# Kernel tuning notes

Hardware: AMD Instinct MI355X
Metric: run time of the kernel (lower is better)

The kernel has to match this reference:

```python
import jax, jax.numpy as jnp
import numpy as np

B, T, D, U, O = 256, 512, 256, 512, 64  # batch, n_steps, feature_in, units, n_output


def setup_inputs() -> dict:
    key = jax.random.key(0)
    k_x, k_wx, k_wh, k_wd = jax.random.split(key, 4)
    x = jax.random.normal(k_x, (B, T, D), dtype=jnp.float32)
    # Lecun-normal-ish init scales so activations stay sane
    Wx = jax.random.normal(k_wx, (D, 4 * U), dtype=jnp.float32) * (1.0 / np.sqrt(D))
    Wh = jax.random.normal(k_wh, (U, 4 * U), dtype=jnp.float32) * (1.0 / np.sqrt(U))
    b = jnp.zeros((4 * U,), dtype=jnp.float32)
    Wd = jax.random.normal(k_wd, (U, O), dtype=jnp.float32) * (1.0 / np.sqrt(U))
    bd = jnp.zeros((O,), dtype=jnp.float32)
    return {"x": x, "Wx": Wx, "Wh": Wh, "b": b, "Wd": Wd, "bd": bd}


def reference(x, Wx, Wh, b, Wd, bd):
    """Sequential LSTM scan (flax nn.LSTMCell math) + per-step dense decode.

    x: [B, T, D] -> y: [B, T, O]
    """
    batch = x.shape[0]
    units = Wh.shape[0]
    c0 = jnp.zeros((batch, units), dtype=x.dtype)
    h0 = jnp.zeros((batch, units), dtype=x.dtype)

    def step(carry, xt):
        c, h = carry
        gates = xt @ Wx + h @ Wh + b            # [B, 4U]
        i, f, g, o = jnp.split(gates, 4, axis=-1)
        i = jax.nn.sigmoid(i)
        f = jax.nn.sigmoid(f)
        g = jnp.tanh(g)
        o = jax.nn.sigmoid(o)
        c_new = f * c + i * g
        h_new = o * jnp.tanh(c_new)
        y = h_new @ Wd + bd                     # [B, O]
        return (c_new, h_new), y

    xs = jnp.swapaxes(x, 0, 1)                  # [T, B, D]
    _, ys = jax.lax.scan(step, (c0, h0), xs)    # ys: [T, B, O]
    return jnp.swapaxes(ys, 0, 1)               # [B, T, O]
```

## Files before the change

kernel.cpp:

```cpp
#include <hip/hip_runtime.h>


#define Bb 256
#define Tt 512
#define Dd 256
#define Uu 512
#define Oo 64

typedef short bs8 __attribute__((ext_vector_type(8)));
typedef float f32x4 __attribute__((ext_vector_type(4)));

__device__ __forceinline__ unsigned short f2bf(float f) {
  unsigned u = __float_as_uint(f);
  u += 0x7fffu + ((u >> 16) & 1u);
  return (unsigned short)(u >> 16);
}
__device__ __forceinline__ float bf2f(unsigned short s) {
  return __uint_as_float(((unsigned)s) << 16);
}
__device__ __forceinline__ float sigm(float v) { return 1.0f / (1.0f + __expf(-v)); }
__device__ __forceinline__ float tanhfast(float v) { return 2.0f / (1.0f + __expf(-2.0f * v)) - 1.0f; }

__device__ __forceinline__ int zbyte(int row, int k) {
  return (row * 1536 + k * 2) ^ ((row & 7) << 4);
}

__global__ void rnn_init_bar(unsigned* bar) {
  __hip_atomic_store(&bar[threadIdx.x], 0u, __ATOMIC_RELAXED, __HIP_MEMORY_SCOPE_AGENT);
}

__launch_bounds__(256, 2)
__global__ void rnn_lstm_kernel(const float* __restrict__ x, const float* __restrict__ Wx,
                                const float* __restrict__ Wh, const float* __restrict__ bias,
                                const float* __restrict__ Wd, const float* __restrict__ bd,
                                float* __restrict__ out, unsigned short* hbuf, unsigned* bar) {
  __shared__ __align__(16) char zs[16 * 768 * 2];
  __shared__ float gates[4][16][17];
  __shared__ float wdl[512][2];
  __shared__ float ypart[16][2][16];

  const int tid = threadIdx.x;
  const int lane = tid & 63;
  const int wid = tid >> 6;
  const int bid = blockIdx.x;
  const int bg = (bid & 7) | ((bid >> 8) << 3);
  const int ug = (bid >> 3) & 31;
  const int b_base = bg * 16;
  const int u_base = ug * 16;
  const int oc0 = ug * 2;

  unsigned* fl = bar + bg * 32;

  bs8 breg[24];
  {
    const int gc = wid * 512 + u_base + (lane & 15);
    const int kfr = (lane >> 4) * 8;
#pragma unroll
    for (int ks = 0; ks < 24; ++ks) {
      bs8 bb;
#pragma unroll
      for (int e = 0; e < 8; ++e) {
        int kg = ks * 32 + kfr + e;
        float w = (kg < 256) ? Wx[(size_t)kg * 2048 + gc]
                             : Wh[(size_t)(kg - 256) * 2048 + gc];
        bb[e] = (short)f2bf(w);
      }
      breg[ks] = bb;
    }
  }

  const int prow = tid & 15;
  const int usec = tid >> 4;
  const int us4 = usec & 3;
  float bi[4], bff[4], bgg[4], boo[4];
  if (tid < 64) {
#pragma unroll
    for (int j = 0; j < 4; ++j) {
      int ugl = u_base + us4 * 4 + j;
      bi[j]  = bias[0 * 512 + ugl];
      bff[j] = bias[1 * 512 + ugl];
      bgg[j] = bias[2 * 512 + ugl];
      boo[j] = bias[3 * 512 + ugl];
    }
  }
  float cst[4] = {0.f, 0.f, 0.f, 0.f};

  union U16 { unsigned long long q[2]; bs8 v; };

#pragma unroll
  for (int i = 0; i < 4; ++i) {
    int c = tid + i * 256;
    int u = c >> 1, oc = c & 1;
    wdl[u][oc] = Wd[(size_t)u * Oo + oc0 + oc];
  }
  {
    int row = tid >> 4;
    int d0 = (tid & 15) * 16;
    const float* xp = x + ((size_t)(b_base + row) * Tt + 0) * Dd + d0;
    float4 v0 = *(const float4*)xp;
    float4 v1 = *(const float4*)(xp + 4);
    float4 v2 = *(const float4*)(xp + 8);
    float4 v3 = *(const float4*)(xp + 12);
    bs8 p0, p1;
    p0[0] = (short)f2bf(v0.x); p0[1] = (short)f2bf(v0.y);
    p0[2] = (short)f2bf(v0.z); p0[3] = (short)f2bf(v0.w);
    p0[4] = (short)f2bf(v1.x); p0[5] = (short)f2bf(v1.y);
    p0[6] = (short)f2bf(v1.z); p0[7] = (short)f2bf(v1.w);
    p1[0] = (short)f2bf(v2.x); p1[1] = (short)f2bf(v2.y);
    p1[2] = (short)f2bf(v2.z); p1[3] = (short)f2bf(v2.w);
    p1[4] = (short)f2bf(v3.x); p1[5] = (short)f2bf(v3.y);
    p1[6] = (short)f2bf(v3.z); p1[7] = (short)f2bf(v3.w);
    *(bs8*)(zs + zbyte(row, d0)) = p0;
    *(bs8*)(zs + zbyte(row, d0 + 8)) = p1;
  }
#pragma unroll
  for (int i = 0; i < 4; ++i) {
    int c = tid + i * 256;
    int row = c >> 6;
    int u0 = (c & 63) * 8;
    bs8 zz = {0, 0, 0, 0, 0, 0, 0, 0};
    *(bs8*)(zs + zbyte(row, 256 + u0)) = zz;
  }
  __syncthreads();

  for (int t = 0; t < Tt; ++t) {
    f32x4 acc0 = {0, 0, 0, 0}, acc1 = {0, 0, 0, 0};
    {
      const int arow = lane & 15;
      const int akf = (lane >> 4) * 8;
#pragma unroll
      for (int ks = 0; ks < 24; ks += 2) {
        bs8 av0 = *(const bs8*)(zs + zbyte(arow, ks * 32 + akf));
        bs8 av1 = *(const bs8*)(zs + zbyte(arow, (ks + 1) * 32 + akf));
        acc0 = __builtin_amdgcn_mfma_f32_16x16x32_bf16(av0, breg[ks], acc0, 0, 0, 0);
        acc1 = __builtin_amdgcn_mfma_f32_16x16x32_bf16(av1, breg[ks + 1], acc1, 0, 0, 0);
      }
      acc0 += acc1;
    }
    {
      const int u16 = lane & 15;
      const int rb = (lane >> 4) * 4;
#pragma unroll
      for (int j = 0; j < 4; ++j) gates[wid][rb + j][u16] = acc0[j];
    }
    __syncthreads();

    if (tid < 64) {
      unsigned long long hpack = 0ull;
#pragma unroll
      for (int j = 0; j < 4; ++j) {
        int u = us4 * 4 + j;
        float gi = gates[0][prow][u] + bi[j];
        float gf = gates[1][prow][u] + bff[j];
        float gg = gates[2][prow][u] + bgg[j];
        float go = gates[3][prow][u] + boo[j];
        float iv = sigm(gi), fv = sigm(gf), gv = tanhfast(gg), ov = sigm(go);
        float cn = fv * cst[j] + iv * gv;
        cst[j] = cn;
        float hv = ov * tanhfast(cn);
        hpack |= ((unsigned long long)f2bf(hv)) << (16 * j);
      }
      unsigned long long* hp =
          (unsigned long long*)(hbuf + (size_t)(t & 1) * Bb * Uu +
                                (size_t)(b_base + prow) * Uu + u_base + us4 * 4);
      unsigned long long old = __hip_atomic_exchange(hp, hpack, __ATOMIC_RELAXED,
                                                     __HIP_MEMORY_SCOPE_AGENT);
      asm volatile("" :: "v"(old));
    }
    __syncthreads();
    if (tid == 0) {
      unsigned oldf = __hip_atomic_exchange(&fl[ug], (unsigned)(t + 1),
                                            __ATOMIC_RELAXED, __HIP_MEMORY_SCOPE_AGENT);
      asm volatile("" :: "v"(oldf));
    }

    if (t + 1 < Tt) {
      int row = tid >> 4;
      int d0 = (tid & 15) * 16;
      const float* xp = x + ((size_t)(b_base + row) * Tt + (t + 1)) * Dd + d0;
      float4 v0 = *(const float4*)xp;
      float4 v1 = *(const float4*)(xp + 4);
      float4 v2 = *(const float4*)(xp + 8);
      float4 v3 = *(const float4*)(xp + 12);
      bs8 p0, p1;
      p0[0] = (short)f2bf(v0.x); p0[1] = (short)f2bf(v0.y);
      p0[2] = (short)f2bf(v0.z); p0[3] = (short)f2bf(v0.w);
      p0[4] = (short)f2bf(v1.x); p0[5] = (short)f2bf(v1.y);
      p0[6] = (short)f2bf(v1.z); p0[7] = (short)f2bf(v1.w);
      p1[0] = (short)f2bf(v2.x); p1[1] = (short)f2bf(v2.y);
      p1[2] = (short)f2bf(v2.z); p1[3] = (short)f2bf(v2.w);
      p1[4] = (short)f2bf(v3.x); p1[5] = (short)f2bf(v3.y);
      p1[6] = (short)f2bf(v3.z); p1[7] = (short)f2bf(v3.w);
      *(bs8*)(zs + zbyte(row, d0)) = p0;
      *(bs8*)(zs + zbyte(row, d0 + 8)) = p1;
    }

    if (t > 0) {
      float s0 = 0.f, s1 = 0.f;
#pragma unroll
      for (int c8 = 0; c8 < 4; ++c8) {
        int k = 256 + usec * 32 + c8 * 8;
        bs8 hv = *(const bs8*)(zs + zbyte(prow, k));
#pragma unroll
        for (int e = 0; e < 8; ++e) {
          float hf = bf2f((unsigned short)hv[e]);
          int u = usec * 32 + c8 * 8 + e;
          s0 += hf * wdl[u][0];
          s1 += hf * wdl[u][1];
        }
      }
      ypart[prow][0][usec] = s0;
      ypart[prow][1][usec] = s1;
    }
    __syncthreads();
    if (t > 0 && tid < 32) {
      int b = tid >> 1, oc = tid & 1;
      float s = bd[oc0 + oc];
#pragma unroll
      for (int q = 0; q < 16; ++q) s += ypart[b][oc][q];
      out[((size_t)(b_base + b) * Tt + (t - 1)) * Oo + oc0 + oc] = s;
    }
    if (wid == 1) {
      unsigned v;
      do {
        v = __hip_atomic_load(&fl[lane & 31], __ATOMIC_RELAXED, __HIP_MEMORY_SCOPE_AGENT);
      } while (__any((int)(v < (unsigned)(t + 1))));
    }
    __builtin_amdgcn_sched_barrier(0);
    __syncthreads();

    {
      const unsigned short* hsrc = hbuf + (size_t)(t & 1) * Bb * Uu;
#pragma unroll
      for (int i = 0; i < 4; ++i) {
        int c = tid + i * 256;
        int row = c >> 6;
        int u0 = (c & 63) * 8;
        const unsigned long long* p =
            (const unsigned long long*)(hsrc + (size_t)(b_base + row) * Uu + u0);
        U16 uu;
        uu.q[0] = __hip_atomic_load(p, __ATOMIC_RELAXED, __HIP_MEMORY_SCOPE_AGENT);
        uu.q[1] = __hip_atomic_load(p + 1, __ATOMIC_RELAXED, __HIP_MEMORY_SCOPE_AGENT);
        *(bs8*)(zs + zbyte(row, 256 + u0)) = uu.v;
      }
    }
    __syncthreads();
  }

  {
    float s0 = 0.f, s1 = 0.f;
#pragma unroll
    for (int c8 = 0; c8 < 4; ++c8) {
      int k = 256 + usec * 32 + c8 * 8;
      bs8 hv = *(const bs8*)(zs + zbyte(prow, k));
#pragma unroll
      for (int e = 0; e < 8; ++e) {
        float hf = bf2f((unsigned short)hv[e]);
        int u = usec * 32 + c8 * 8 + e;
        s0 += hf * wdl[u][0];
        s1 += hf * wdl[u][1];
      }
    }
    ypart[prow][0][usec] = s0;
    ypart[prow][1][usec] = s1;
    __syncthreads();
    if (tid < 32) {
      int b = tid >> 1, oc = tid & 1;
      float s = bd[oc0 + oc];
#pragma unroll
      for (int q = 0; q < 16; ++q) s += ypart[b][oc][q];
      out[((size_t)(b_base + b) * Tt + (Tt - 1)) * Oo + oc0 + oc] = s;
    }
  }
}

extern "C" void kernel_launch(void* const* d_in, const int* in_sizes, int n_in,
                              void* d_out, int out_size, void* d_ws, size_t ws_size,
                              hipStream_t stream) {
  const float* x  = (const float*)d_in[0];
  const float* Wx = (const float*)d_in[1];
  const float* Wh = (const float*)d_in[2];
  const float* bs = (const float*)d_in[3];
  const float* Wd = (const float*)d_in[4];
  const float* bd = (const float*)d_in[5];
  float* out = (float*)d_out;

  unsigned short* hbuf = (unsigned short*)d_ws;
  unsigned* bar = (unsigned*)((char*)d_ws + (size_t)2 * Bb * Uu * 2);

  rnn_init_bar<<<1, 512, 0, stream>>>(bar);
  rnn_lstm_kernel<<<dim3(512), dim3(256), 0, stream>>>(x, Wx, Wh, bs, Wd, bd, out, hbuf, bar);
}
```

Measured before the change: 2.409 ms.

## Precompute next step's input projection during barrier wait and split flag polling across waves

The x·Wx part of the gate MFMA (first 8 k-slices) for step t+1 is now computed after the h exchange wait, off the recurrent critical path, and carried into the next iteration as an accumulator seed. Every wave now polls its own slice of the flags instead of a single wave, which removes one __syncthreads. The h-load pattern is remapped so each lane loads two rows of 16 contiguous elements. The cost is extra registers for the carried accumulators and a different global/LDS access pattern.

```diff
diff --git a/kernel.cpp b/kernel.cpp
--- a/kernel.cpp
+++ b/kernel.cpp
@@ -84,8 +84,6 @@
     }
   }
   float cst[4] = {0.f, 0.f, 0.f, 0.f};
-
-  union U16 { unsigned long long q[2]; bs8 v; };
 
 #pragma unroll
   for (int i = 0; i < 4; ++i) {
@@ -123,20 +121,30 @@
   }
   __syncthreads();
 
+  const int arow = lane & 15;
+  const int akf = (lane >> 4) * 8;
+  f32x4 accx0 = {0, 0, 0, 0}, accx1 = {0, 0, 0, 0};
+#pragma unroll
+  for (int ks = 0; ks < 8; ks += 2) {
+    bs8 av0 = *(const bs8*)(zs + zbyte(arow, ks * 32 + akf));
+    bs8 av1 = *(const bs8*)(zs + zbyte(arow, (ks + 1) * 32 + akf));
+    accx0 = __builtin_amdgcn_mfma_f32_16x16x32_bf16(av0, breg[ks], accx0, 0, 0, 0);
+    accx1 = __builtin_amdgcn_mfma_f32_16x16x32_bf16(av1, breg[ks + 1], accx1, 0, 0, 0);
+  }
+
+  const int cp = wid * 8 + (lane >> 3);
+  const int ca = lane & 7;
+
   for (int t = 0; t < Tt; ++t) {
-    f32x4 acc0 = {0, 0, 0, 0}, acc1 = {0, 0, 0, 0};
-    {
-      const int arow = lane & 15;
-      const int akf = (lane >> 4) * 8;
-#pragma unroll
-      for (int ks = 0; ks < 24; ks += 2) {
-        bs8 av0 = *(const bs8*)(zs + zbyte(arow, ks * 32 + akf));
-        bs8 av1 = *(const bs8*)(zs + zbyte(arow, (ks + 1) * 32 + akf));
-        acc0 = __builtin_amdgcn_mfma_f32_16x16x32_bf16(av0, breg[ks], acc0, 0, 0, 0);
-        acc1 = __builtin_amdgcn_mfma_f32_16x16x32_bf16(av1, breg[ks + 1], acc1, 0, 0, 0);
-      }
-      acc0 += acc1;
-    }
+    f32x4 acc0 = accx0, acc1 = accx1;
+#pragma unroll
+    for (int ks = 8; ks < 24; ks += 2) {
+      bs8 av0 = *(const bs8*)(zs + zbyte(arow, ks * 32 + akf));
+      bs8 av1 = *(const bs8*)(zs + zbyte(arow, (ks + 1) * 32 + akf));
+      acc0 = __builtin_amdgcn_mfma_f32_16x16x32_bf16(av0, breg[ks], acc0, 0, 0, 0);
+      acc1 = __builtin_amdgcn_mfma_f32_16x16x32_bf16(av1, breg[ks + 1], acc1, 0, 0, 0);
+    }
+    acc0 += acc1;
     {
       const int u16 = lane & 15;
       const int rb = (lane >> 4) * 4;
@@ -194,7 +202,6 @@
       *(bs8*)(zs + zbyte(row, d0)) = p0;
       *(bs8*)(zs + zbyte(row, d0 + 8)) = p1;
     }
-
     if (t > 0) {
       float s0 = 0.f, s1 = 0.f;
 #pragma unroll
@@ -213,6 +220,42 @@
       ypart[prow][1][usec] = s1;
     }
     __syncthreads();
+
+    const unsigned short* hsrc = hbuf + (size_t)(t & 1) * Bb * Uu;
+    {
+      unsigned v;
+      do {
+        v = __hip_atomic_load(&fl[wid * 8 + (lane & 7)], __ATOMIC_RELAXED,
+                              __HIP_MEMORY_SCOPE_AGENT);
+      } while (__any((int)(v < (unsigned)(t + 1))));
+    }
+    __builtin_amdgcn_sched_barrier(0);
+    unsigned long long cd0, cd1, cd2, cd3, cd4, cd5, cd6, cd7;
+    {
+      const unsigned long long* p0 = (const unsigned long long*)
+          (hsrc + (size_t)(b_base + ca * 2) * Uu + cp * 16);
+      const unsigned long long* p1 = (const unsigned long long*)
+          (hsrc + (size_t)(b_base + ca * 2 + 1) * Uu + cp * 16);
+      cd0 = __hip_atomic_load(p0 + 0, __ATOMIC_RELAXED, __HIP_MEMORY_SCOPE_AGENT);
+      cd1 = __hip_atomic_load(p0 + 1, __ATOMIC_RELAXED, __HIP_MEMORY_SCOPE_AGENT);
+      cd2 = __hip_atomic_load(p0 + 2, __ATOMIC_RELAXED, __HIP_MEMORY_SCOPE_AGENT);
+      cd3 = __hip_atomic_load(p0 + 3, __ATOMIC_RELAXED, __HIP_MEMORY_SCOPE_AGENT);
+      cd4 = __hip_atomic_load(p1 + 0, __ATOMIC_RELAXED, __HIP_MEMORY_SCOPE_AGENT);
+      cd5 = __hip_atomic_load(p1 + 1, __ATOMIC_RELAXED, __HIP_MEMORY_SCOPE_AGENT);
+      cd6 = __hip_atomic_load(p1 + 2, __ATOMIC_RELAXED, __HIP_MEMORY_SCOPE_AGENT);
+      cd7 = __hip_atomic_load(p1 + 3, __ATOMIC_RELAXED, __HIP_MEMORY_SCOPE_AGENT);
+    }
+    if (t + 1 < Tt) {
+      f32x4 ax0 = {0, 0, 0, 0}, ax1 = {0, 0, 0, 0};
+#pragma unroll
+      for (int ks = 0; ks < 8; ks += 2) {
+        bs8 av0 = *(const bs8*)(zs + zbyte(arow, ks * 32 + akf));
+        bs8 av1 = *(const bs8*)(zs + zbyte(arow, (ks + 1) * 32 + akf));
+        ax0 = __builtin_amdgcn_mfma_f32_16x16x32_bf16(av0, breg[ks], ax0, 0, 0, 0);
+        ax1 = __builtin_amdgcn_mfma_f32_16x16x32_bf16(av1, breg[ks + 1], ax1, 0, 0, 0);
+      }
+      accx0 = ax0; accx1 = ax1;
+    }
     if (t > 0 && tid < 32) {
       int b = tid >> 1, oc = tid & 1;
       float s = bd[oc0 + oc];
@@ -220,29 +263,16 @@
       for (int q = 0; q < 16; ++q) s += ypart[b][oc][q];
       out[((size_t)(b_base + b) * Tt + (t - 1)) * Oo + oc0 + oc] = s;
     }
-    if (wid == 1) {
-      unsigned v;
-      do {
-        v = __hip_atomic_load(&fl[lane & 31], __ATOMIC_RELAXED, __HIP_MEMORY_SCOPE_AGENT);
-      } while (__any((int)(v < (unsigned)(t + 1))));
-    }
-    __builtin_amdgcn_sched_barrier(0);
-    __syncthreads();
-
     {
-      const unsigned short* hsrc = hbuf + (size_t)(t & 1) * Bb * Uu;
-#pragma unroll
-      for (int i = 0; i < 4; ++i) {
-        int c = tid + i * 256;
-        int row = c >> 6;
-        int u0 = (c & 63) * 8;
-        const unsigned long long* p =
-            (const unsigned long long*)(hsrc + (size_t)(b_base + row) * Uu + u0);
-        U16 uu;
-        uu.q[0] = __hip_atomic_load(p, __ATOMIC_RELAXED, __HIP_MEMORY_SCOPE_AGENT);
-        uu.q[1] = __hip_atomic_load(p + 1, __ATOMIC_RELAXED, __HIP_MEMORY_SCOPE_AGENT);
-        *(bs8*)(zs + zbyte(row, 256 + u0)) = uu.v;
-      }
+      int r0 = ca * 2, r1 = ca * 2 + 1;
+      *(unsigned long long*)(zs + zbyte(r0, 256 + cp * 16 + 0))  = cd0;
+      *(unsigned long long*)(zs + zbyte(r0, 256 + cp * 16 + 4))  = cd1;
+      *(unsigned long long*)(zs + zbyte(r0, 256 + cp * 16 + 8))  = cd2;
+      *(unsigned long long*)(zs + zbyte(r0, 256 + cp * 16 + 12)) = cd3;
+      *(unsigned long long*)(zs + zbyte(r1, 256 + cp * 16 + 0))  = cd4;
+      *(unsigned long long*)(zs + zbyte(r1, 256 + cp * 16 + 4))  = cd5;
+      *(unsigned long long*)(zs + zbyte(r1, 256 + cp * 16 + 8))  = cd6;
+      *(unsigned long long*)(zs + zbyte(r1, 256 + cp * 16 + 12)) = cd7;
     }
     __syncthreads();
   }
@@ -263,14 +293,14 @@
     }
     ypart[prow][0][usec] = s0;
     ypart[prow][1][usec] = s1;
-    __syncthreads();
-    if (tid < 32) {
-      int b = tid >> 1, oc = tid & 1;
-      float s = bd[oc0 + oc];
-#pragma unroll
-      for (int q = 0; q < 16; ++q) s += ypart[b][oc][q];
-      out[((size_t)(b_base + b) * Tt + (Tt - 1)) * Oo + oc0 + oc] = s;
-    }
+  }
+  __syncthreads();
+  if (tid < 32) {
+    int b = tid >> 1, oc = tid & 1;
+    float s = bd[oc0 + oc];
+#pragma unroll
+    for (int q = 0; q < 16; ++q) s += ypart[b][oc][q];
+    out[((size_t)(b_base + b) * Tt + (Tt - 1)) * Oo + oc0 + oc] = s;
   }
 }
 
```

After: 2.735 ms. 13.6% more time.
